# Kernel optimization log

Measured on AMD Instinct MI355X. Metric: run time of the kernel, lower is better.

Reference implementation:

```python
import jax, jax.numpy as jnp
import numpy as np

B, C, H, W = 4, 8, 64, 64
C8 = C // 8  # = 1, required for the residual broadcast in PAM


def _conv1x1(x, w, b):
    # x: [B,C,H,W], w: [O,C], b: [O] -> [B,O,H,W]
    return jnp.einsum('bchw,oc->bohw', x, w) + b[None, :, None, None]


def setup_inputs() -> dict:
    key = jax.random.key(0)
    ks = jax.random.split(key, 13)
    s_c = 1.0 / np.sqrt(C)
    inp = {'x': jax.random.normal(ks[0], (B, C, H, W), jnp.float32)}
    # CAM: three 1x1 convs C->C
    inp['cam_wq'] = jax.random.normal(ks[1], (C, C), jnp.float32) * s_c
    inp['cam_bq'] = jnp.zeros((C,), jnp.float32)
    inp['cam_wk'] = jax.random.normal(ks[2], (C, C), jnp.float32) * s_c
    inp['cam_bk'] = jnp.zeros((C,), jnp.float32)
    inp['cam_wv'] = jax.random.normal(ks[3], (C, C), jnp.float32) * s_c
    inp['cam_bv'] = jnp.zeros((C,), jnp.float32)
    # PAM: three 1x1 convs C->C//8
    inp['pam_wq'] = jax.random.normal(ks[4], (C8, C), jnp.float32) * s_c
    inp['pam_bq'] = jnp.zeros((C8,), jnp.float32)
    inp['pam_wk'] = jax.random.normal(ks[5], (C8, C), jnp.float32) * s_c
    inp['pam_bk'] = jnp.zeros((C8,), jnp.float32)
    inp['pam_wv'] = jax.random.normal(ks[6], (C8, C), jnp.float32) * s_c
    inp['pam_bv'] = jnp.zeros((C8,), jnp.float32)
    return inp


def reference(x, cam_wq, cam_bq, cam_wk, cam_bk, cam_wv, cam_bv,
              pam_wq, pam_bq, pam_wk, pam_bk, pam_wv, pam_bv):
    b, c, h, w = x.shape
    hw = h * w

    # ---- Channel Attention Module (C x C attention) ----
    q = _conv1x1(x, cam_wq, cam_bq).reshape(b, c, hw)            # [B,C,HW]
    k = _conv1x1(x, cam_wk, cam_bk).reshape(b, c, hw)            # [B,C,HW]
    v = _conv1x1(x, cam_wv, cam_bv).reshape(b, c, hw)            # [B,C,HW]
    attn_c = jax.nn.softmax(jnp.einsum('bcn,bdn->bcd', q, k), axis=-1)  # [B,C,C]
    out_cam = jnp.einsum('bcd,bdn->bcn', attn_c, v).reshape(b, c, h, w) + x

    # ---- Pixel Attention Module (HW x HW attention, C//8 channels) ----
    pq = _conv1x1(x, pam_wq, pam_bq).reshape(b, -1, hw)          # [B,C8,HW]
    pk = _conv1x1(x, pam_wk, pam_bk).reshape(b, -1, hw)          # [B,C8,HW]
    pv = _conv1x1(x, pam_wv, pam_bv).reshape(b, -1, hw)          # [B,C8,HW]
    attn_p = jax.nn.softmax(jnp.einsum('bcn,bcm->bnm', pq, pk), axis=-1)  # [B,HW,HW]
    # out = v @ attn^T  -> [B,C8,HW]; residual broadcasts C8=1 against C
    out_p = jnp.einsum('bcm,bnm->bcn', pv, attn_p).reshape(b, c // 8, h, w)
    out_pam = out_p + x                                          # broadcast [B,1,H,W]+[B,C,H,W]

    return out_pam + out_cam
```

## Files before the change

### kernel.cpp

```cpp
#include <hip/hip_runtime.h>

#define CC 8
#define HW 4096
#define L2E 1.4426950408889634f

typedef __attribute__((ext_vector_type(4))) float f32x4;
typedef __attribute__((ext_vector_type(2))) float f32x2;

static __device__ __forceinline__ float dpp_sum64(float v) {
#define DPPSTEP(CTRL, RM, BM)                                              \
  v += __int_as_float(__builtin_amdgcn_update_dpp(                         \
      0, __float_as_int(v), CTRL, RM, BM, true));
  DPPSTEP(0x111, 0xf, 0xf)
  DPPSTEP(0x112, 0xf, 0xf)
  DPPSTEP(0x114, 0xf, 0xe)
  DPPSTEP(0x118, 0xf, 0xc)
  DPPSTEP(0x142, 0xa, 0xf)
  DPPSTEP(0x143, 0xc, 0xf)
#undef DPPSTEP
  return v;
}

static __device__ __forceinline__ void step2(f32x2 kk, f32x2 vv, f32x2 aa,
                                             f32x2& dd, f32x2& nn) {
  f32x2 arg = aa * kk;
  f32x2 ee;
  ee[0] = __builtin_amdgcn_exp2f(arg[0]);
  ee[1] = __builtin_amdgcn_exp2f(arg[1]);
  dd += ee;
  nn = __builtin_elementwise_fma(ee, vv, nn);
}

__global__ __launch_bounds__(512) void kFused(
    const float* __restrict__ x,
    const float* __restrict__ cwq, const float* __restrict__ cbq,
    const float* __restrict__ cwk, const float* __restrict__ cbk,
    const float* __restrict__ cwv, const float* __restrict__ cbv,
    const float* __restrict__ pwq, const float* __restrict__ pbq,
    const float* __restrict__ pwk, const float* __restrict__ pbk,
    const float* __restrict__ pwv, const float* __restrict__ pbv,
    float* __restrict__ out)
{
  const int b = blockIdx.x >> 6, tile = blockIdx.x & 63;
  const int n0 = tile * 64;
  const int t = threadIdx.x, ln = t & 63;
  const int wid = __builtin_amdgcn_readfirstlane(t >> 6);

  __shared__ __align__(16) float k2s[HW];
  __shared__ __align__(16) float pvs[HW];
  __shared__ float redd[8][64], redn[8][64];
  __shared__ float gpart[8][44];
  __shared__ float sums[44], Gl[64], Ll[64], Al[64], Mp[64], cvs[8], outp[64];

  const float* xb = x + b * CC * HW;

  f32x4 xa[CC], xc[CC];
  {
    const int m8 = t * 8;
    #pragma unroll
    for (int c = 0; c < CC; ++c) {
      xa[c] = *(const f32x4*)(xb + c * HW + m8);
      xc[c] = *(const f32x4*)(xb + c * HW + m8 + 4);
    }
    f32x4 ka, kb, va, vb;
    #pragma unroll
    for (int j = 0; j < 8; ++j) {
      float kk = pbk[0], vv = pbv[0];
      #pragma unroll
      for (int c = 0; c < CC; ++c) {
        const float xv = (j < 4) ? xa[c][j & 3] : xc[c][j & 3];
        kk = fmaf(pwk[c], xv, kk);
        vv = fmaf(pwv[c], xv, vv);
      }
      kk *= L2E;
      if (j < 4) { ka[j] = kk; va[j] = vv; }
      else       { kb[j & 3] = kk; vb[j & 3] = vv; }
    }
    ((f32x4*)k2s)[t * 2 + 0] = ka;
    ((f32x4*)k2s)[t * 2 + 1] = kb;
    ((f32x4*)pvs)[t * 2 + 0] = va;
    ((f32x4*)pvs)[t * 2 + 1] = vb;
  }

  {
    float acc[44];
    #pragma unroll
    for (int i = 0; i < 44; ++i) acc[i] = 0.f;
    #pragma unroll
    for (int j = 0; j < 8; ++j) {
      float xv[CC];
      #pragma unroll
      for (int c = 0; c < CC; ++c) xv[c] = (j < 4) ? xa[c][j & 3] : xc[c][j & 3];
      int k = 0;
      #pragma unroll
      for (int c = 0; c < CC; ++c) {
        #pragma unroll
        for (int d = c; d < CC; ++d) { acc[k] = fmaf(xv[c], xv[d], acc[k]); ++k; }
      }
      #pragma unroll
      for (int c = 0; c < CC; ++c) acc[36 + c] += xv[c];
    }
    #pragma unroll
    for (int i = 0; i < 44; ++i) acc[i] = dpp_sum64(acc[i]);
    if (ln == 63) {
      #pragma unroll
      for (int i = 0; i < 44; ++i) gpart[wid][i] = acc[i];
    }
  }

  float xn[CC];
  #pragma unroll
  for (int c = 0; c < CC; ++c) xn[c] = xb[c * HW + n0 + ln];
  float a = pbq[0];
  #pragma unroll
  for (int c = 0; c < CC; ++c) a = fmaf(pwq[c], xn[c], a);

  __syncthreads();

  {
    const f32x4* kp = ((const f32x4*)k2s) + (wid << 7);
    const f32x4* vp = ((const f32x4*)pvs) + (wid << 7);
    f32x2 aa; aa[0] = a; aa[1] = a;
    f32x2 z; z[0] = 0.f; z[1] = 0.f;
    f32x2 dA = z, dB = z, dC = z, dD = z;
    f32x2 nA = z, nB = z, nC = z, nD = z;
    #pragma unroll 2
    for (int i = 0; i < 128; i += 2) {
      const f32x4 k4a = kp[i], k4b = kp[i + 1];
      const f32x4 v4a = vp[i], v4b = vp[i + 1];
      f32x2 kk, vv;
      kk[0] = k4a[0]; kk[1] = k4a[1]; vv[0] = v4a[0]; vv[1] = v4a[1];
      step2(kk, vv, aa, dA, nA);
      kk[0] = k4a[2]; kk[1] = k4a[3]; vv[0] = v4a[2]; vv[1] = v4a[3];
      step2(kk, vv, aa, dB, nB);
      kk[0] = k4b[0]; kk[1] = k4b[1]; vv[0] = v4b[0]; vv[1] = v4b[1];
      step2(kk, vv, aa, dC, nC);
      kk[0] = k4b[2]; kk[1] = k4b[3]; vv[0] = v4b[2]; vv[1] = v4b[3];
      step2(kk, vv, aa, dD, nD);
    }
    const f32x2 dS = (dA + dB) + (dC + dD);
    const f32x2 nS = (nA + nB) + (nC + nD);
    redd[wid][ln] = dS[0] + dS[1];
    redn[wid][ln] = nS[0] + nS[1];
  }
  __syncthreads();

  if (t < 64) {
    float D = 0.f, N = 0.f;
    #pragma unroll
    for (int s = 0; s < 8; ++s) { D += redd[s][t]; N += redn[s][t]; }
    outp[t] = N / D;
  }
  if (t < 44) {
    float s = 0.f;
    #pragma unroll
    for (int w = 0; w < 8; ++w) s += gpart[w][t];
    sums[t] = s;
  }
  __syncthreads();

  const int c = ln >> 3, d = ln & 7;
  if (t < 64) {
    const int lo = min(c, d), hi = max(c, d);
    Gl[t] = sums[lo * 8 + hi - lo * (lo + 1) / 2];
  }
  __syncthreads();

  float Lv = 0.f;
  if (t < 64) {
    float qs = 0.f, ks = 0.f;
    #pragma unroll
    for (int e = 0; e < 8; ++e) {
      qs = fmaf(cwq[c * 8 + e], sums[36 + e], qs);
      ks = fmaf(cwk[d * 8 + e], sums[36 + e], ks);
    }
    float A = 0.f;
    #pragma unroll
    for (int e = 0; e < 8; ++e) {
      float inner = 0.f;
      #pragma unroll
      for (int f = 0; f < 8; ++f) inner = fmaf(Gl[e * 8 + f], cwk[d * 8 + f], inner);
      A = fmaf(cwq[c * 8 + e], inner, A);
    }
    Lv = A + qs * cbk[d] + cbq[c] * ks + 4096.f * cbq[c] * cbk[d];
    Ll[t] = Lv;
  }
  __syncthreads();

  if (t < 64) {
    float mx = -INFINITY;
    #pragma unroll
    for (int f = 0; f < 8; ++f) mx = fmaxf(mx, Ll[c * 8 + f]);
    float ssum = 0.f;
    #pragma unroll
    for (int f = 0; f < 8; ++f) ssum += __expf(Ll[c * 8 + f] - mx);
    Al[t] = __expf(Lv - mx) / ssum;
  }
  __syncthreads();

  if (t < 64) {
    float M = 0.f;
    #pragma unroll
    for (int f = 0; f < 8; ++f) M = fmaf(Al[c * 8 + f], cwv[f * 8 + d], M);
    if (d == c) M += 2.f;
    Mp[t] = M;
    if (d == 0) {
      float cvv = 0.f;
      #pragma unroll
      for (int f = 0; f < 8; ++f) cvv = fmaf(Al[c * 8 + f], cbv[f], cvv);
      cvs[c] = cvv;
    }
  }
  __syncthreads();

  {
    float o = cvs[wid] + outp[ln];
    #pragma unroll
    for (int dd = 0; dd < 8; ++dd) o = fmaf(Mp[wid * 8 + dd], xn[dd], o);
    out[(b * 8 + wid) * HW + n0 + ln] = o;
  }
}

extern "C" void kernel_launch(void* const* d_in, const int* in_sizes, int n_in,
                              void* d_out, int out_size, void* d_ws, size_t ws_size,
                              hipStream_t stream) {
  const float* x   = (const float*)d_in[0];
  const float* cwq = (const float*)d_in[1];
  const float* cbq = (const float*)d_in[2];
  const float* cwk = (const float*)d_in[3];
  const float* cbk = (const float*)d_in[4];
  const float* cwv = (const float*)d_in[5];
  const float* cbv = (const float*)d_in[6];
  const float* pwq = (const float*)d_in[7];
  const float* pbq = (const float*)d_in[8];
  const float* pwk = (const float*)d_in[9];
  const float* pbk = (const float*)d_in[10];
  const float* pwv = (const float*)d_in[11];
  const float* pbv = (const float*)d_in[12];
  float* out = (float*)d_out;

  hipLaunchKernelGGL(kFused, dim3(256), dim3(512), 0, stream,
                     x, cwq, cbq, cwk, cbk, cwv, cbv,
                     pwq, pbq, pwk, pbk, pwv, pbv, out);
}
```

Baseline: 20.63 us.

## Halve pixel tile per block and split key range across half-waves

Each block now handles 32 query pixels instead of 64, and the grid doubles to 512 blocks. Within a wave, the two 32-lane halves each take half of that wave's key slice, so each thread does half as many exp/FMA steps in the attention loop. Partial sums from both halves are added during the final reduction. The per-block prologue, which computes the K/V projections and Gram sums over all 4096 pixels, is now repeated by twice as many blocks. A min-occupancy launch bound is added, which may restrict registers and cause spills.

After: 24.10 us. +16.8%, slower.

```diff
diff --git a/kernel.cpp b/kernel.cpp
--- a/kernel.cpp
+++ b/kernel.cpp
@@ -31,7 +31,7 @@
   nn = __builtin_elementwise_fma(ee, vv, nn);
 }
 
-__global__ __launch_bounds__(512) void kFused(
+__global__ __launch_bounds__(512, 4) void kFused(
     const float* __restrict__ x,
     const float* __restrict__ cwq, const float* __restrict__ cbq,
     const float* __restrict__ cwk, const float* __restrict__ cbk,
@@ -41,16 +41,18 @@
     const float* __restrict__ pwv, const float* __restrict__ pbv,
     float* __restrict__ out)
 {
-  const int b = blockIdx.x >> 6, tile = blockIdx.x & 63;
-  const int n0 = tile * 64;
+  const int b = blockIdx.x >> 7;
+  const int n0 = (blockIdx.x & 127) * 32;
   const int t = threadIdx.x, ln = t & 63;
   const int wid = __builtin_amdgcn_readfirstlane(t >> 6);
+  const int px = ln & 31;
+  const int mh = ln >> 5;
 
   __shared__ __align__(16) float k2s[HW];
   __shared__ __align__(16) float pvs[HW];
   __shared__ float redd[8][64], redn[8][64];
   __shared__ float gpart[8][44];
-  __shared__ float sums[44], Gl[64], Ll[64], Al[64], Mp[64], cvs[8], outp[64];
+  __shared__ float sums[44], Gl[64], Ll[64], Al[64], Mp[64], cvs[8], outp[32];
 
   const float* xb = x + b * CC * HW;
 
@@ -110,7 +112,7 @@
 
   float xn[CC];
   #pragma unroll
-  for (int c = 0; c < CC; ++c) xn[c] = xb[c * HW + n0 + ln];
+  for (int c = 0; c < CC; ++c) xn[c] = xb[c * HW + n0 + px];
   float a = pbq[0];
   #pragma unroll
   for (int c = 0; c < CC; ++c) a = fmaf(pwq[c], xn[c], a);
@@ -118,37 +120,34 @@
   __syncthreads();
 
   {
-    const f32x4* kp = ((const f32x4*)k2s) + (wid << 7);
-    const f32x4* vp = ((const f32x4*)pvs) + (wid << 7);
+    const f32x4* kp = ((const f32x4*)k2s) + (wid << 7) + (mh << 6);
+    const f32x4* vp = ((const f32x4*)pvs) + (wid << 7) + (mh << 6);
     f32x2 aa; aa[0] = a; aa[1] = a;
     f32x2 z; z[0] = 0.f; z[1] = 0.f;
-    f32x2 dA = z, dB = z, dC = z, dD = z;
-    f32x2 nA = z, nB = z, nC = z, nD = z;
-    #pragma unroll 2
-    for (int i = 0; i < 128; i += 2) {
-      const f32x4 k4a = kp[i], k4b = kp[i + 1];
-      const f32x4 v4a = vp[i], v4b = vp[i + 1];
+    f32x2 dA = z, dB = z, nA = z, nB = z;
+    #pragma unroll 4
+    for (int i = 0; i < 64; ++i) {
+      const f32x4 k4 = kp[i], v4 = vp[i];
       f32x2 kk, vv;
-      kk[0] = k4a[0]; kk[1] = k4a[1]; vv[0] = v4a[0]; vv[1] = v4a[1];
+      kk[0] = k4[0]; kk[1] = k4[1]; vv[0] = v4[0]; vv[1] = v4[1];
       step2(kk, vv, aa, dA, nA);
-      kk[0] = k4a[2]; kk[1] = k4a[3]; vv[0] = v4a[2]; vv[1] = v4a[3];
+      kk[0] = k4[2]; kk[1] = k4[3]; vv[0] = v4[2]; vv[1] = v4[3];
       step2(kk, vv, aa, dB, nB);
-      kk[0] = k4b[0]; kk[1] = k4b[1]; vv[0] = v4b[0]; vv[1] = v4b[1];
-      step2(kk, vv, aa, dC, nC);
-      kk[0] = k4b[2]; kk[1] = k4b[3]; vv[0] = v4b[2]; vv[1] = v4b[3];
-      step2(kk, vv, aa, dD, nD);
-    }
-    const f32x2 dS = (dA + dB) + (dC + dD);
-    const f32x2 nS = (nA + nB) + (nC + nD);
+    }
+    const f32x2 dS = dA + dB;
+    const f32x2 nS = nA + nB;
     redd[wid][ln] = dS[0] + dS[1];
     redn[wid][ln] = nS[0] + nS[1];
   }
   __syncthreads();
 
-  if (t < 64) {
+  if (t < 32) {
     float D = 0.f, N = 0.f;
     #pragma unroll
-    for (int s = 0; s < 8; ++s) { D += redd[s][t]; N += redn[s][t]; }
+    for (int s = 0; s < 8; ++s) {
+      D += redd[s][t] + redd[s][t + 32];
+      N += redn[s][t] + redn[s][t + 32];
+    }
     outp[t] = N / D;
   }
   if (t < 44) {
@@ -213,11 +212,12 @@
   }
   __syncthreads();
 
-  {
-    float o = cvs[wid] + outp[ln];
-    #pragma unroll
-    for (int dd = 0; dd < 8; ++dd) o = fmaf(Mp[wid * 8 + dd], xn[dd], o);
-    out[(b * 8 + wid) * HW + n0 + ln] = o;
+  if (t < 256) {
+    const int ch = t >> 5, p = t & 31;
+    float o = cvs[ch] + outp[p];
+    #pragma unroll
+    for (int dd = 0; dd < 8; ++dd) o = fmaf(Mp[ch * 8 + dd], xn[dd], o);
+    out[(b * 8 + ch) * HW + n0 + p] = o;
   }
 }
 
@@ -239,7 +239,7 @@
   const float* pbv = (const float*)d_in[12];
   float* out = (float*)d_out;
 
-  hipLaunchKernelGGL(kFused, dim3(256), dim3(512), 0, stream,
+  hipLaunchKernelGGL(kFused, dim3(512), dim3(512), 0, stream,
                      x, cwq, cbq, cwk, cbk, cwv, cbv,
                      pwq, pbq, pwk, pbk, pwv, pbv, out);
 }
```

## Keep PAM keys and values in registers and rotate queries across the wave

Applied to the files above, without the earlier changes.

Each thread now keeps its 8 PAM key/value pairs in registers instead of writing them to LDS and streaming the wave's keys back. The query and the running softmax sums are rotated around the 64 lanes with a DPP wave rotate, so after 64 steps every query has seen all of the wave's keys. The aim is to drop the LDS stores and loads and one block barrier. In exchange, each step adds three cross-lane DPP ops, and the den/num accumulation becomes a serial chain through the rotation, which may expose latency.

Measured after the change: 20.40 us. Within noise of the previous version (-1.1%).

```diff
diff --git a/kernel.cpp b/kernel.cpp
--- a/kernel.cpp
+++ b/kernel.cpp
@@ -19,6 +19,11 @@
   DPPSTEP(0x143, 0xc, 0xf)
 #undef DPPSTEP
   return v;
+}
+
+static __device__ __forceinline__ float wave_ror1(float v) {
+  return __int_as_float(__builtin_amdgcn_update_dpp(
+      0, __float_as_int(v), 0x13C , 0xF, 0xF, true));
 }
 
 static __device__ __forceinline__ void step2(f32x2 kk, f32x2 vv, f32x2 aa,
@@ -46,8 +51,6 @@
   const int t = threadIdx.x, ln = t & 63;
   const int wid = __builtin_amdgcn_readfirstlane(t >> 6);
 
-  __shared__ __align__(16) float k2s[HW];
-  __shared__ __align__(16) float pvs[HW];
   __shared__ float redd[8][64], redn[8][64];
   __shared__ float gpart[8][44];
   __shared__ float sums[44], Gl[64], Ll[64], Al[64], Mp[64], cvs[8], outp[64];
@@ -55,6 +58,7 @@
   const float* xb = x + b * CC * HW;
 
   f32x4 xa[CC], xc[CC];
+  f32x4 ka, kb, va, vb;
   {
     const int m8 = t * 8;
     #pragma unroll
@@ -62,7 +66,6 @@
       xa[c] = *(const f32x4*)(xb + c * HW + m8);
       xc[c] = *(const f32x4*)(xb + c * HW + m8 + 4);
     }
-    f32x4 ka, kb, va, vb;
     #pragma unroll
     for (int j = 0; j < 8; ++j) {
       float kk = pbk[0], vv = pbv[0];
@@ -76,10 +79,6 @@
       if (j < 4) { ka[j] = kk; va[j] = vv; }
       else       { kb[j & 3] = kk; vb[j & 3] = vv; }
     }
-    ((f32x4*)k2s)[t * 2 + 0] = ka;
-    ((f32x4*)k2s)[t * 2 + 1] = kb;
-    ((f32x4*)pvs)[t * 2 + 0] = va;
-    ((f32x4*)pvs)[t * 2 + 1] = vb;
   }
 
   {
@@ -115,33 +114,30 @@
   #pragma unroll
   for (int c = 0; c < CC; ++c) a = fmaf(pwq[c], xn[c], a);
 
-  __syncthreads();
-
-  {
-    const f32x4* kp = ((const f32x4*)k2s) + (wid << 7);
-    const f32x4* vp = ((const f32x4*)pvs) + (wid << 7);
-    f32x2 aa; aa[0] = a; aa[1] = a;
-    f32x2 z; z[0] = 0.f; z[1] = 0.f;
-    f32x2 dA = z, dB = z, dC = z, dD = z;
-    f32x2 nA = z, nB = z, nC = z, nD = z;
-    #pragma unroll 2
-    for (int i = 0; i < 128; i += 2) {
-      const f32x4 k4a = kp[i], k4b = kp[i + 1];
-      const f32x4 v4a = vp[i], v4b = vp[i + 1];
+  {
+    float den = 0.f, num = 0.f;
+    #pragma unroll 4
+    for (int r = 0; r < 64; ++r) {
+      f32x2 aa; aa[0] = a; aa[1] = a;
+      f32x2 dd; dd[0] = 0.f; dd[1] = 0.f;
+      f32x2 nn = dd;
       f32x2 kk, vv;
-      kk[0] = k4a[0]; kk[1] = k4a[1]; vv[0] = v4a[0]; vv[1] = v4a[1];
-      step2(kk, vv, aa, dA, nA);
-      kk[0] = k4a[2]; kk[1] = k4a[3]; vv[0] = v4a[2]; vv[1] = v4a[3];
-      step2(kk, vv, aa, dB, nB);
-      kk[0] = k4b[0]; kk[1] = k4b[1]; vv[0] = v4b[0]; vv[1] = v4b[1];
-      step2(kk, vv, aa, dC, nC);
-      kk[0] = k4b[2]; kk[1] = k4b[3]; vv[0] = v4b[2]; vv[1] = v4b[3];
-      step2(kk, vv, aa, dD, nD);
-    }
-    const f32x2 dS = (dA + dB) + (dC + dD);
-    const f32x2 nS = (nA + nB) + (nC + nD);
-    redd[wid][ln] = dS[0] + dS[1];
-    redn[wid][ln] = nS[0] + nS[1];
+      kk[0] = ka[0]; kk[1] = ka[1]; vv[0] = va[0]; vv[1] = va[1];
+      step2(kk, vv, aa, dd, nn);
+      kk[0] = ka[2]; kk[1] = ka[3]; vv[0] = va[2]; vv[1] = va[3];
+      step2(kk, vv, aa, dd, nn);
+      kk[0] = kb[0]; kk[1] = kb[1]; vv[0] = vb[0]; vv[1] = vb[1];
+      step2(kk, vv, aa, dd, nn);
+      kk[0] = kb[2]; kk[1] = kb[3]; vv[0] = vb[2]; vv[1] = vb[3];
+      step2(kk, vv, aa, dd, nn);
+      den += dd[0] + dd[1];
+      num += nn[0] + nn[1];
+      a   = wave_ror1(a);
+      den = wave_ror1(den);
+      num = wave_ror1(num);
+    }
+    redd[wid][ln] = den;
+    redn[wid][ln] = num;
   }
   __syncthreads();
 
@@ -216,7 +212,7 @@
   {
     float o = cvs[wid] + outp[ln];
     #pragma unroll
-    for (int dd = 0; dd < 8; ++dd) o = fmaf(Mp[wid * 8 + dd], xn[dd], o);
+    for (int dd2 = 0; dd2 < 8; ++dd2) o = fmaf(Mp[wid * 8 + dd2], xn[dd2], o);
     out[(b * 8 + wid) * HW + n0 + ln] = o;
   }
 }
```
